# Kernel optimization log

Measured on AMD Instinct MI355X. Metric: run time of the kernel, lower is better.

## Reference

```python
import jax, jax.numpy as jnp
import numpy as np

N = 100000
D = 512   # input_size
C = 2     # output_class
QDIM = 128


def setup_inputs() -> dict:
    key = jax.random.key(0)
    ks = jax.random.split(key, 12)
    s = 0.02
    return {
        "feats": jax.random.normal(ks[0], (N, D), jnp.float32),
        "c": jax.random.normal(ks[1], (N, C), jnp.float32),
        "single_predictions": jax.random.normal(ks[2], (N, 1), jnp.float32),
        # self.lin = Linear(D, D) + ReLU
        "W_lin": jax.random.normal(ks[3], (D, D), jnp.float32) * s,
        "b_lin": jnp.zeros((D,), jnp.float32),
        # self.q = Linear(D, 128) + Tanh
        "W_q": jax.random.normal(ks[4], (QDIM, D), jnp.float32) * s,
        "b_q": jnp.zeros((QDIM,), jnp.float32),
        # self.v = Dropout(0.0) + Linear(D, D)
        "W_v": jax.random.normal(ks[5], (D, D), jnp.float32) * s,
        "b_v": jnp.zeros((D,), jnp.float32),
        # self.fcc = Conv1d(C, C, kernel_size=D)
        "W_fcc": jax.random.normal(ks[6], (C, C, D), jnp.float32) * s,
        "b_fcc": jnp.zeros((C,), jnp.float32),
    }


def reference(feats, c, single_predictions, W_lin, b_lin, W_q, b_q, W_v, b_v, W_fcc, b_fcc):
    n = feats.shape[0]
    k = int(0.2 * n)

    preds = single_predictions[:, 0]                      # [N]
    # torch.topk(largest=False): indices of the k smallest; zero them out
    _, lastk_idx = jax.lax.top_k(-preds, k)
    preds = preds.at[lastk_idx].set(0.0)
    instance_score = jax.nn.softmax(preds, axis=0)[:, None]  # [N,1], softmax over instances

    f = feats * instance_score + feats                    # [N,D]
    f = jax.nn.relu(f @ W_lin.T + b_lin)                  # self.lin
    V = f @ W_v.T + b_v                                   # [N,D] (dropout p=0)
    Q = jnp.tanh(f @ W_q.T + b_q)                         # [N,128]

    # torch.sort(c, 0, descending)[1][0,:] == per-class argmax over instances
    m_indices = jnp.argmax(c, axis=0)                     # [C]
    m_feats = f[m_indices]                                # [C,D]
    q_max = jnp.tanh(m_feats @ W_q.T + b_q)               # [C,128]

    A = Q @ q_max.T                                       # [N,C]
    A = jax.nn.softmax(A / jnp.sqrt(jnp.float32(QDIM)), axis=0)  # softmax over instances
    B = A.T @ V                                           # [C,D]

    # Conv1d(C, C, kernel=D) on B[None] -> length-1 output: full contraction
    Cout = jnp.einsum('id,oid->o', B, W_fcc) + b_fcc      # [C]
    return Cout[None, :], A, B
```

## Files before the change

kernel.cpp:

```cpp
#include <hip/hip_runtime.h>
#include <stdint.h>

typedef unsigned short u16;
typedef __bf16 bf16t;
typedef bf16t bf16x8 __attribute__((ext_vector_type(8)));
typedef float f32x4 __attribute__((ext_vector_type(4)));
typedef unsigned long long ull;

#define NROWS 100000
#define DD 512
#define QD 128
#define KSEL 20000
#define NB 1563

__device__ __forceinline__ uint32_t fmono(float x){
  uint32_t u = __float_as_uint(x);
  return (u & 0x80000000u) ? ~u : (u | 0x80000000u);
}
__device__ __forceinline__ float finv(uint32_t k){
  uint32_t u = (k & 0x80000000u) ? (k & 0x7fffffffu) : ~k;
  return __uint_as_float(u);
}
__device__ __forceinline__ u16 f2bf(float x){
  uint32_t u = __float_as_uint(x);
  u += 0x7fffu + ((u >> 16) & 1u);
  return (u16)(u >> 16);
}
__device__ __forceinline__ uint32_t pkbf(float a, float b){
  return (uint32_t)f2bf(a) | ((uint32_t)f2bf(b) << 16);
}

struct Scal {
  uint32_t keyT;
  float Z;
  uint32_t pad[14];
};

#define MFMA16(A,B,C) __builtin_amdgcn_mfma_f32_16x16x32_bf16(A,B,C,0,0,0)

__global__ void k_conv(const float* __restrict__ Wl, const float* __restrict__ Wv,
                       const float* __restrict__ Wq, u16* __restrict__ wch,
                       uint32_t* __restrict__ hist, ull* __restrict__ cmax){
  int idx = blockIdx.x*256 + threadIdx.x;
  if (idx < 65536) hist[idx] = 0u;
  if (idx == 0){ cmax[0] = 0ull; cmax[1] = 0ull; }
  int ci  = idx >> 12;
  int rem = idx & 4095;
  int r   = rem >> 5;
  int col = rem & 31;
  float v;
  if (ci < 64){
    int nt = ci >> 4, kc = ci & 15;
    v = Wl[(size_t)(nt*128 + r)*DD + kc*32 + col];
  } else {
    int c2 = ci - 64;
    int nt2 = c2 >> 4, kc = c2 & 15;
    if (nt2 == 0) v = Wq[(size_t)r*DD + kc*32 + col];
    else          v = Wv[(size_t)((nt2-1)*128 + r)*DD + kc*32 + col];
  }
  wch[idx] = f2bf(v);
}

__global__ void k_sel1(const float* __restrict__ preds, const float* __restrict__ c,
                       uint32_t* __restrict__ hist, ull* __restrict__ cmax){
  __shared__ ull kr0[4], kr1[4];
  const int t = threadIdx.x;
  const int gid = blockIdx.x*256 + t;
  const int lane = t & 63;

  const float4* p4 = (const float4*)preds;
  for (int i = gid; i < 25000; i += 65536){
    float4 v = p4[i];
    atomicAdd(&hist[fmono(v.x) >> 16], 1u);
    atomicAdd(&hist[fmono(v.y) >> 16], 1u);
    atomicAdd(&hist[fmono(v.z) >> 16], 1u);
    atomicAdd(&hist[fmono(v.w) >> 16], 1u);
  }

  ull k0 = 0ull, k1 = 0ull;
  const float4* c4 = (const float4*)c;
  for (int i = gid; i < 50000; i += 65536){
    float4 v = c4[i];
    uint32_t r0 = 2u*i, r1 = 2u*i + 1u;
    ull a0 = ((ull)fmono(v.x) << 32) | (ull)(~r0);
    ull a1 = ((ull)fmono(v.z) << 32) | (ull)(~r1);
    ull b0 = ((ull)fmono(v.y) << 32) | (ull)(~r0);
    ull b1 = ((ull)fmono(v.w) << 32) | (ull)(~r1);
    if (a0 > k0) k0 = a0;
    if (a1 > k0) k0 = a1;
    if (b0 > k1) k1 = b0;
    if (b1 > k1) k1 = b1;
  }
  #pragma unroll
  for (int off = 32; off; off >>= 1){
    ull o0 = __shfl_xor(k0, off); if (o0 > k0) k0 = o0;
    ull o1 = __shfl_xor(k1, off); if (o1 > k1) k1 = o1;
  }
  if (lane == 0){ kr0[t >> 6] = k0; kr1[t >> 6] = k1; }
  __syncthreads();
  if (t == 0){
    ull m0 = kr0[0], m1 = kr1[0];
    #pragma unroll
    for (int w = 1; w < 4; ++w){
      if (kr0[w] > m0) m0 = kr0[w];
      if (kr1[w] > m1) m1 = kr1[w];
    }
    atomicMax(&cmax[0], m0);
    atomicMax(&cmax[1], m1);
  }
}

#define CAND_CAP 8192
__launch_bounds__(1024)
__global__ void k_prep2(const float* __restrict__ preds,
                        const uint32_t* __restrict__ hist,
                        Scal* __restrict__ sc){
  __shared__ uint32_t cand[CAND_CAP];
  __shared__ uint32_t wsum[16], woff[16];
  __shared__ float zred[16];
  __shared__ uint32_t s_B, s_cumBelow, s_keyT, candN;
  const int t = threadIdx.x;
  const int lane = t & 63, wv = t >> 6;

  if (t == 0) candN = 0;

  const int b0 = t*64;
  uint32_t local = 0;
  {
    const uint4* h4 = (const uint4*)(hist + b0);
    #pragma unroll 4
    for (int q = 0; q < 16; ++q){ uint4 hv = h4[q]; local += hv.x + hv.y + hv.z + hv.w; }
  }
  uint32_t x = local;
  #pragma unroll
  for (int off = 1; off < 64; off <<= 1){
    uint32_t y = __shfl_up(x, off);
    if (lane >= off) x += y;
  }
  if (lane == 63) wsum[wv] = x;
  __syncthreads();
  if (t == 0){
    uint32_t cum = 0;
    for (int w = 0; w < 16; ++w){ woff[w] = cum; cum += wsum[w]; }
  }
  __syncthreads();
  uint32_t excl = x - local + woff[wv];
  if (excl < KSEL && excl + local >= KSEL){
    uint32_t cum = excl;
    for (int b = 0; b < 64; ++b){
      uint32_t h = hist[b0 + b];
      if (cum + h >= KSEL){ s_B = (uint32_t)(b0 + b); s_cumBelow = cum; break; }
      cum += h;
    }
  }
  __syncthreads();
  const uint32_t B = s_B;

  float sA = 0.f;
  const float4* p4 = (const float4*)preds;
  for (int i = t; i < 25000; i += 1024){
    float4 v = p4[i];
    float vv[4] = {v.x, v.y, v.z, v.w};
    #pragma unroll
    for (int e = 0; e < 4; ++e){
      uint32_t k = fmono(vv[e]);
      uint32_t bb = k >> 16;
      if (bb > B){
        sA += __expf(vv[e]);
      } else if (bb == B){
        uint32_t idx = atomicAdd(&candN, 1u);
        if (idx < CAND_CAP) cand[idx] = k;
      }
    }
  }
  #pragma unroll
  for (int off = 32; off; off >>= 1) sA += __shfl_xor(sA, off);
  if (lane == 0) zred[wv] = sA;
  __syncthreads();

  const uint32_t n = candN < CAND_CAP ? candN : CAND_CAP;
  const uint32_t r = KSEL - s_cumBelow;
  for (uint32_t i = t; i < n; i += 1024){
    uint32_t ki = cand[i];
    uint32_t less = 0, eq = 0;
    for (uint32_t j = 0; j < n; ++j){
      uint32_t kj = cand[j];
      less += (kj < ki) ? 1u : 0u;
      eq   += (kj == ki) ? 1u : 0u;
    }
    if (less < r && r <= less + eq) s_keyT = ki;
  }
  __syncthreads();
  const uint32_t keyT = s_keyT;

  float sCA = 0.f;
  for (uint32_t i = t; i < n; i += 1024){
    uint32_t k = cand[i];
    if (k > keyT) sCA += __expf(finv(k));
  }
  #pragma unroll
  for (int off = 32; off; off >>= 1) sCA += __shfl_xor(sCA, off);
  if (lane == 0) zred[wv] += sCA;
  __syncthreads();
  if (t == 0){
    float Z = (float)KSEL;
    for (int w = 0; w < 16; ++w) Z += zred[w];
    sc->keyT = keyT; sc->Z = Z;
  }
}

__global__ void k_prep3(const float* __restrict__ preds, const float* __restrict__ feats,
                        const float* __restrict__ Wl, const float* __restrict__ bl,
                        const ull* __restrict__ cmax, const Scal* __restrict__ sc,
                        float* __restrict__ fmFw){
  __shared__ float fmX[2][512];
  __shared__ uint32_t s_mi[2];
  const int t = threadIdx.x;
  if (t < 2) s_mi[t] = ~(uint32_t)(cmax[t] & 0xffffffffull);
  __syncthreads();
  for (int i = t; i < 1024; i += 256){
    int j = i >> 9, col = i & 511;
    fmX[j][col] = feats[(size_t)s_mi[j]*DD + col];
  }
  __syncthreads();
  const int nn = blockIdx.x*32 + (t >> 3);
  const int h = t & 7;
  const float4* wr4 = (const float4*)(Wl + (size_t)nn*DD + h*64);
  const float4* x04 = (const float4*)(&fmX[0][h*64]);
  const float4* x14 = (const float4*)(&fmX[1][h*64]);
  float a0 = 0.f, a1 = 0.f;
  #pragma unroll
  for (int k = 0; k < 16; ++k){
    float4 w = wr4[k], u = x04[k], v = x14[k];
    a0 += u.x*w.x + u.y*w.y + u.z*w.z + u.w*w.w;
    a1 += v.x*w.x + v.y*w.y + v.z*w.z + v.w*w.w;
  }
  a0 += __shfl_xor(a0, 1); a0 += __shfl_xor(a0, 2); a0 += __shfl_xor(a0, 4);
  a1 += __shfl_xor(a1, 1); a1 += __shfl_xor(a1, 2); a1 += __shfl_xor(a1, 4);
  if (h == 0){
    uint32_t keyT = sc->keyT;
    float Z = sc->Z;
    float p0 = preds[s_mi[0]]; float q0 = (fmono(p0) <= keyT) ? 0.f : p0;
    float g0 = 1.f + __expf(q0) / Z;
    float p1 = preds[s_mi[1]]; float q1 = (fmono(p1) <= keyT) ? 0.f : p1;
    float g1 = 1.f + __expf(q1) / Z;
    float v0 = bl[nn] + g0*a0; fmFw[nn]       = v0 > 0.f ? v0 : 0.f;
    float v1 = bl[nn] + g1*a1; fmFw[512 + nn] = v1 > 0.f ? v1 : 0.f;
  }
}

__global__ void k_prep4(const float* __restrict__ Wq, const float* __restrict__ bq,
                        const float* __restrict__ fmFw, float* __restrict__ qmv){
  __shared__ float xs[512];
  const int t = threadIdx.x;
  const int j = blockIdx.x;
  for (int i = t; i < 512; i += 256) xs[i] = fmFw[j*512 + i];
  __syncthreads();
  const int q = t >> 1, h = t & 1;
  const float4* wr4 = (const float4*)(Wq + (size_t)q*DD + h*256);
  const float4* x4  = (const float4*)(&xs[h*256]);
  float a = 0.f;
  #pragma unroll 4
  for (int k = 0; k < 64; ++k){
    float4 w = wr4[k], u = x4[k];
    a += u.x*w.x + u.y*w.y + u.z*w.z + u.w*w.w;
  }
  a += __shfl_xor(a, 1);
  if (h == 0) qmv[j*QD + q] = tanhf(bq[q] + a);
}

__launch_bounds__(256, 2)
__global__ void k_fused(const float* __restrict__ feats, const float* __restrict__ preds,
                        const u16* __restrict__ wch,
                        const float* __restrict__ bl, const float* __restrict__ bv,
                        const float* __restrict__ bq, const float* __restrict__ qmv,
                        const Scal* __restrict__ sc,
                        float* __restrict__ gpart, float* __restrict__ gpartE,
                        float* __restrict__ Aout){
  __shared__ __align__(16) u16 AF[32768];
  __shared__ __align__(16) float sred[512];
  const int tid = threadIdx.x;
  const int lane = tid & 63, quad = lane >> 4, l16 = lane & 15;
  const int wave = tid >> 6;
  const long i0 = (long)blockIdx.x * 64;
  const uint32_t keyT = sc->keyT;
  const float Z = sc->Z;

  const u16* bsrc = wch + (size_t)((wave*32 + l16)*32 + quad*8);
  uint4 pA0 = *(const uint4*)(bsrc);
  uint4 pA1 = *(const uint4*)(bsrc + 512);
  uint4 pB0 = *(const uint4*)(bsrc + 4096);
  uint4 pB1 = *(const uint4*)(bsrc + 4096 + 512);

  {
    int row = lane;
    long ir = i0 + row; if (ir >= NROWS) ir = NROWS - 1;
    float p = preds[ir];
    float pm = (fmono(p) <= keyT) ? 0.f : p;
    float g = 1.f + __expf(pm) / Z;
    const float4* src = (const float4*)(feats + ir*DD + wave*128);
    u16* dstrow = AF + row*512;
    const int swz = row & 7;
    #pragma unroll
    for (int j = 0; j < 16; ++j){
      float4 a = src[2*j], b = src[2*j + 1];
      uint4 pk;
      pk.x = pkbf(a.x*g, a.y*g); pk.y = pkbf(a.z*g, a.w*g);
      pk.z = pkbf(b.x*g, b.y*g); pk.w = pkbf(b.z*g, b.w*g);
      int blk = (wave << 4) | j;
      *(uint4*)&dstrow[(blk ^ swz) << 3] = pk;
    }
  }
  __syncthreads();

  const int sb = l16 & 7;
  f32x4 acc[4][2];
  uint32_t pkF[4][16];
  float eR0[4][4], eR1[4][4];
  int ci = 0;

#define KSTEP(P0, P1)                                                              \
  {                                                                                \
    bf16x8 b0 = __builtin_bit_cast(bf16x8, P0);                                    \
    bf16x8 b1 = __builtin_bit_cast(bf16x8, P1);                                    \
    if (ci + 2 < 144){                                                             \
      const u16* s_ = bsrc + (size_t)(ci + 2)*4096;                                \
      P0 = *(const uint4*)s_;                                                      \
      P1 = *(const uint4*)(s_ + 512);                                              \
    }                                                                              \
    int abk = ((((ci & 15) << 2) | quad) ^ sb) << 3;                               \
    bf16x8 a0 = *(const bf16x8*)&AF[(     l16)*512 + abk];                         \
    bf16x8 a1 = *(const bf16x8*)&AF[(16 + l16)*512 + abk];                         \
    bf16x8 a2 = *(const bf16x8*)&AF[(32 + l16)*512 + abk];                         \
    bf16x8 a3 = *(const bf16x8*)&AF[(48 + l16)*512 + abk];                         \
    acc[0][0] = MFMA16(a0, b0, acc[0][0]);                                         \
    acc[0][1] = MFMA16(a0, b1, acc[0][1]);                                         \
    acc[1][0] = MFMA16(a1, b0, acc[1][0]);                                         \
    acc[1][1] = MFMA16(a1, b1, acc[1][1]);                                         \
    acc[2][0] = MFMA16(a2, b0, acc[2][0]);                                         \
    acc[2][1] = MFMA16(a2, b1, acc[2][1]);                                         \
    acc[3][0] = MFMA16(a3, b0, acc[3][0]);                                         \
    acc[3][1] = MFMA16(a3, b1, acc[3][1]);                                         \
    ++ci;                                                                          \
  }

  for (int nt = 0; nt < 4; ++nt){
    #pragma unroll
    for (int mi = 0; mi < 4; ++mi)
      #pragma unroll
      for (int ni = 0; ni < 2; ++ni) acc[mi][ni] = (f32x4){0.f,0.f,0.f,0.f};
    for (int kh = 0; kh < 8; ++kh){
      KSTEP(pA0, pA1);
      KSTEP(pB0, pB1);
    }
    #pragma unroll
    for (int ni = 0; ni < 2; ++ni){
      float bb = bl[nt*128 + wave*32 + ni*16 + l16];
      #pragma unroll
      for (int mi = 0; mi < 4; ++mi){
        float e0 = acc[mi][ni][0] + bb; e0 = e0 > 0.f ? e0 : 0.f;
        float e1 = acc[mi][ni][1] + bb; e1 = e1 > 0.f ? e1 : 0.f;
        float e2 = acc[mi][ni][2] + bb; e2 = e2 > 0.f ? e2 : 0.f;
        float e3 = acc[mi][ni][3] + bb; e3 = e3 > 0.f ? e3 : 0.f;
        pkF[nt][mi*4 + ni*2 + 0] = pkbf(e0, e1);
        pkF[nt][mi*4 + ni*2 + 1] = pkbf(e2, e3);
      }
    }
  }

  __syncthreads();
  #pragma unroll
  for (int nt = 0; nt < 4; ++nt)
    #pragma unroll
    for (int mi = 0; mi < 4; ++mi)
      #pragma unroll
      for (int ni = 0; ni < 2; ++ni){
        int col = nt*128 + wave*32 + ni*16 + l16;
        int r0 = mi*16 + quad*4;
        uint32_t x = pkF[nt][mi*4 + ni*2], y = pkF[nt][mi*4 + ni*2 + 1];
        int cb = col >> 3, cw = col & 7;
        AF[(r0+0)*512 + ((cb ^ ((r0+0)&7)) << 3) + cw] = (u16)x;
        AF[(r0+1)*512 + ((cb ^ ((r0+1)&7)) << 3) + cw] = (u16)(x >> 16);
        AF[(r0+2)*512 + ((cb ^ ((r0+2)&7)) << 3) + cw] = (u16)y;
        AF[(r0+3)*512 + ((cb ^ ((r0+3)&7)) << 3) + cw] = (u16)(y >> 16);
      }
  __syncthreads();

  for (int nt2 = 0; nt2 < 5; ++nt2){
    #pragma unroll
    for (int mi = 0; mi < 4; ++mi)
      #pragma unroll
      for (int ni = 0; ni < 2; ++ni) acc[mi][ni] = (f32x4){0.f,0.f,0.f,0.f};
    for (int kh = 0; kh < 8; ++kh){
      KSTEP(pA0, pA1);
      KSTEP(pB0, pB1);
    }
    if (nt2 == 0){
      float p0[4][4], p1[4][4];
      #pragma unroll
      for (int mi = 0; mi < 4; ++mi)
        #pragma unroll
        for (int e = 0; e < 4; ++e){ p0[mi][e] = 0.f; p1[mi][e] = 0.f; }
      #pragma unroll
      for (int ni = 0; ni < 2; ++ni){
        int qc = wave*32 + ni*16 + l16;
        float bqv = bq[qc], q0 = qmv[qc], q1 = qmv[QD + qc];
        #pragma unroll
        for (int mi = 0; mi < 4; ++mi)
          #pragma unroll
          for (int e = 0; e < 4; ++e){
            float tq = tanhf(acc[mi][ni][e] + bqv);
            p0[mi][e] += tq * q0;
            p1[mi][e] += tq * q1;
          }
      }
      #pragma unroll
      for (int off = 1; off <= 8; off <<= 1)
        #pragma unroll
        for (int mi = 0; mi < 4; ++mi)
          #pragma unroll
          for (int e = 0; e < 4; ++e){
            p0[mi][e] += __shfl_xor(p0[mi][e], off);
            p1[mi][e] += __shfl_xor(p1[mi][e], off);
          }
      if (l16 == 0){
        #pragma unroll
        for (int mi = 0; mi < 4; ++mi)
          #pragma unroll
          for (int e = 0; e < 4; ++e){
            int row = mi*16 + quad*4 + e;
            sred[row*8 + 0*4 + wave] = p0[mi][e];
            sred[row*8 + 1*4 + wave] = p1[mi][e];
          }
      }
      __syncthreads();
      #pragma unroll
      for (int mi = 0; mi < 4; ++mi)
        #pragma unroll
        for (int e = 0; e < 4; ++e){
          int row = mi*16 + quad*4 + e;
          bool valid = (i0 + row) < NROWS;
          float sv0 = (sred[row*8+0] + sred[row*8+1] + sred[row*8+2] + sred[row*8+3]) * 0.08838834764831845f;
          float sv1 = (sred[row*8+4] + sred[row*8+5] + sred[row*8+6] + sred[row*8+7]) * 0.08838834764831845f;
          eR0[mi][e] = valid ? __expf(sv0) : 0.f;
          eR1[mi][e] = valid ? __expf(sv1) : 0.f;
        }
      if (tid < 128){
        int row = tid >> 1, j = tid & 1;
        float sv = (sred[row*8 + j*4+0] + sred[row*8 + j*4+1] + sred[row*8 + j*4+2] + sred[row*8 + j*4+3])
                   * 0.08838834764831845f;
        bool valid = (i0 + row) < NROWS;
        float ev = valid ? __expf(sv) : 0.f;
        if (valid) Aout[(i0 + row)*2 + j] = ev;
        float t2 = ev;
        #pragma unroll
        for (int off = 2; off <= 32; off <<= 1) t2 += __shfl_xor(t2, off);
        if (lane < 2) gpartE[(size_t)blockIdx.x*4 + (tid >> 6)*2 + j] = t2;
      }
    } else {
      #pragma unroll
      for (int ni = 0; ni < 2; ++ni){
        int colv = (nt2 - 1)*128 + wave*32 + ni*16 + l16;
        float bvv = bv[colv];
        float b0 = 0.f, b1 = 0.f;
        #pragma unroll
        for (int mi = 0; mi < 4; ++mi)
          #pragma unroll
          for (int e = 0; e < 4; ++e){
            float v = acc[mi][ni][e] + bvv;
            b0 += v * eR0[mi][e];
            b1 += v * eR1[mi][e];
          }
        b0 += __shfl_xor(b0, 16); b0 += __shfl_xor(b0, 32);
        b1 += __shfl_xor(b1, 16); b1 += __shfl_xor(b1, 32);
        if (quad == 0){
          gpart[(size_t)blockIdx.x*1024 + colv]       = b0;
          gpart[(size_t)blockIdx.x*1024 + 512 + colv] = b1;
        }
      }
    }
  }
#undef KSTEP
}

__global__ void k_red(const float* __restrict__ gpart, const float* __restrict__ gpartE,
                      float* __restrict__ sumEV, float* __restrict__ sumE){
  const int t = threadIdx.x;
  if (blockIdx.x == 256){
    __shared__ float r0[256], r1[256];
    float s0 = 0.f, s1 = 0.f;
    for (int i = t; i < NB*2; i += 256){ s0 += gpartE[(size_t)i*2]; s1 += gpartE[(size_t)i*2 + 1]; }
    r0[t] = s0; r1[t] = s1;
    __syncthreads();
    for (int st = 128; st; st >>= 1){
      if (t < st){ r0[t] += r0[t + st]; r1[t] += r1[t + st]; }
      __syncthreads();
    }
    if (t == 0){ sumE[0] = r0[0]; sumE[1] = r1[0]; }
    return;
  }
  __shared__ float4 red[256];
  int col4 = blockIdx.x * 4;
  float4 s = {0.f, 0.f, 0.f, 0.f};
  for (int r = t; r < NB; r += 256){
    float4 v = *(const float4*)(gpart + (size_t)r*1024 + col4);
    s.x += v.x; s.y += v.y; s.z += v.z; s.w += v.w;
  }
  red[t] = s;
  __syncthreads();
  for (int st = 128; st; st >>= 1){
    if (t < st){
      float4 o = red[t + st];
      red[t].x += o.x; red[t].y += o.y; red[t].z += o.z; red[t].w += o.w;
    }
    __syncthreads();
  }
  if (t == 0) *(float4*)(sumEV + col4) = red[0];
}

__global__ void k_post(float* __restrict__ out, const float* __restrict__ sumE,
                       const float* __restrict__ sumEV, const float* __restrict__ Wfcc,
                       const float* __restrict__ bfcc){
  if (blockIdx.x < 782){
    int idx = blockIdx.x*256 + threadIdx.x;
    if (idx < 200000) out[2 + idx] = out[2 + idx] / sumE[idx & 1];
    return;
  }
  __shared__ float red[512];
  int t = threadIdx.x;
  float z0 = sumE[0], z1 = sumE[1];
  float c0 = 0.f, c1 = 0.f;
  for (int e = t; e < 1024; e += 256){
    float bvv = sumEV[e] / ((e >> 9) ? z1 : z0);
    out[200002 + e] = bvv;
    c0 += bvv * Wfcc[e];
    c1 += bvv * Wfcc[1024 + e];
  }
  red[t] = c0; red[256 + t] = c1;
  __syncthreads();
  for (int s = 128; s; s >>= 1){
    if (t < s){ red[t] += red[t + s]; red[256 + t] += red[256 + t + s]; }
    __syncthreads();
  }
  if (t == 0){ out[0] = red[0] + bfcc[0]; out[1] = red[256] + bfcc[1]; }
}

extern "C" void kernel_launch(void* const* d_in, const int* in_sizes, int n_in,
                              void* d_out, int out_size, void* d_ws, size_t ws_size,
                              hipStream_t stream){
  (void)in_sizes; (void)n_in; (void)out_size; (void)ws_size;
  const float* feats = (const float*)d_in[0];
  const float* c     = (const float*)d_in[1];
  const float* preds = (const float*)d_in[2];
  const float* W_lin = (const float*)d_in[3];
  const float* b_lin = (const float*)d_in[4];
  const float* W_q   = (const float*)d_in[5];
  const float* b_q   = (const float*)d_in[6];
  const float* W_v   = (const float*)d_in[7];
  const float* b_v   = (const float*)d_in[8];
  const float* W_fcc = (const float*)d_in[9];
  const float* b_fcc = (const float*)d_in[10];
  float* out = (float*)d_out;
  char* ws = (char*)d_ws;

  u16*   wch    = (u16*)(ws + 0);
  Scal*  sc     = (Scal*)(ws + 1179648);
  float* qmv    = (float*)(ws + 1179712);
  float* sumE   = (float*)(ws + 1180736);
  float* sumEV  = (float*)(ws + 1180800);
  float* fmFw   = (float*)(ws + 1184896);
  float* gpartE = (float*)(ws + 1188992);
  float* gpart  = (float*)(ws + 1214080);
  uint32_t* hist = (uint32_t*)(ws + 1214080);
  ull*      cmax = (ull*)(ws + 1214080 + 262144);

  k_conv <<<2304, 256, 0, stream>>>(W_lin, W_v, W_q, wch, hist, cmax);
  k_sel1 <<<256, 256, 0, stream>>>(preds, c, hist, cmax);
  k_prep2<<<1, 1024, 0, stream>>>(preds, hist, sc);
  k_prep3<<<16, 256, 0, stream>>>(preds, feats, W_lin, b_lin, cmax, sc, fmFw);
  k_prep4<<<2, 256, 0, stream>>>(W_q, b_q, fmFw, qmv);
  k_fused<<<NB, 256, 0, stream>>>(feats, preds, wch, b_lin, b_v, b_q,
                                  qmv, sc, gpart, gpartE, out + 2);
  k_red  <<<257, 256, 0, stream>>>(gpart, gpartE, sumEV, sumE);
  k_post <<<783, 256, 0, stream>>>(out, sumE, sumEV, W_fcc, b_fcc);
}
```

Baseline: 603.6 us.

## Split fused kernel across eight waves and coarsen selection histogram to 4096 bins

```diff
diff --git a/kernel.cpp b/kernel.cpp
--- a/kernel.cpp
+++ b/kernel.cpp
@@ -12,6 +12,7 @@
 #define QD 128
 #define KSEL 20000
 #define NB 1563
+#define NBINS 4096
 
 __device__ __forceinline__ uint32_t fmono(float x){
   uint32_t u = __float_as_uint(x);
@@ -42,7 +43,7 @@
                        const float* __restrict__ Wq, u16* __restrict__ wch,
                        uint32_t* __restrict__ hist, ull* __restrict__ cmax){
   int idx = blockIdx.x*256 + threadIdx.x;
-  if (idx < 65536) hist[idx] = 0u;
+  if (idx < NBINS) hist[idx] = 0u;
   if (idx == 0){ cmax[0] = 0ull; cmax[1] = 0ull; }
   int ci  = idx >> 12;
   int rem = idx & 4095;
@@ -71,10 +72,10 @@
   const float4* p4 = (const float4*)preds;
   for (int i = gid; i < 25000; i += 65536){
     float4 v = p4[i];
-    atomicAdd(&hist[fmono(v.x) >> 16], 1u);
-    atomicAdd(&hist[fmono(v.y) >> 16], 1u);
-    atomicAdd(&hist[fmono(v.z) >> 16], 1u);
-    atomicAdd(&hist[fmono(v.w) >> 16], 1u);
+    atomicAdd(&hist[fmono(v.x) >> 20], 1u);
+    atomicAdd(&hist[fmono(v.y) >> 20], 1u);
+    atomicAdd(&hist[fmono(v.z) >> 20], 1u);
+    atomicAdd(&hist[fmono(v.w) >> 20], 1u);
   }
 
   ull k0 = 0ull, k1 = 0ull;
@@ -124,13 +125,9 @@
 
   if (t == 0) candN = 0;
 
-  const int b0 = t*64;
-  uint32_t local = 0;
-  {
-    const uint4* h4 = (const uint4*)(hist + b0);
-    #pragma unroll 4
-    for (int q = 0; q < 16; ++q){ uint4 hv = h4[q]; local += hv.x + hv.y + hv.z + hv.w; }
-  }
+  const int b0 = t*4;
+  uint4 hv = ((const uint4*)hist)[t];
+  uint32_t local = hv.x + hv.y + hv.z + hv.w;
   uint32_t x = local;
   #pragma unroll
   for (int off = 1; off < 64; off <<= 1){
@@ -147,10 +144,11 @@
   uint32_t excl = x - local + woff[wv];
   if (excl < KSEL && excl + local >= KSEL){
     uint32_t cum = excl;
-    for (int b = 0; b < 64; ++b){
-      uint32_t h = hist[b0 + b];
-      if (cum + h >= KSEL){ s_B = (uint32_t)(b0 + b); s_cumBelow = cum; break; }
-      cum += h;
+    uint32_t hh[4] = {hv.x, hv.y, hv.z, hv.w};
+    #pragma unroll
+    for (int b = 0; b < 4; ++b){
+      if (cum + hh[b] >= KSEL){ s_B = (uint32_t)(b0 + b); s_cumBelow = cum; break; }
+      cum += hh[b];
     }
   }
   __syncthreads();
@@ -164,7 +162,7 @@
     #pragma unroll
     for (int e = 0; e < 4; ++e){
       uint32_t k = fmono(vv[e]);
-      uint32_t bb = k >> 16;
+      uint32_t bb = k >> 20;
       if (bb > B){
         sA += __expf(vv[e]);
       } else if (bb == B){
@@ -269,7 +267,7 @@
   if (h == 0) qmv[j*QD + q] = tanhf(bq[q] + a);
 }
 
-__launch_bounds__(256, 2)
+__launch_bounds__(512, 4)
 __global__ void k_fused(const float* __restrict__ feats, const float* __restrict__ preds,
                         const u16* __restrict__ wch,
                         const float* __restrict__ bl, const float* __restrict__ bv,
@@ -281,12 +279,12 @@
   __shared__ __align__(16) float sred[512];
   const int tid = threadIdx.x;
   const int lane = tid & 63, quad = lane >> 4, l16 = lane & 15;
-  const int wave = tid >> 6;
+  const int wave = tid >> 6, wm = wave >> 2, wn = wave & 3;
   const long i0 = (long)blockIdx.x * 64;
   const uint32_t keyT = sc->keyT;
   const float Z = sc->Z;
 
-  const u16* bsrc = wch + (size_t)((wave*32 + l16)*32 + quad*8);
+  const u16* bsrc = wch + (size_t)((wn*32 + l16)*32 + quad*8);
   uint4 pA0 = *(const uint4*)(bsrc);
   uint4 pA1 = *(const uint4*)(bsrc + 512);
   uint4 pB0 = *(const uint4*)(bsrc + 4096);
@@ -298,66 +296,64 @@
     float p = preds[ir];
     float pm = (fmono(p) <= keyT) ? 0.f : p;
     float g = 1.f + __expf(pm) / Z;
-    const float4* src = (const float4*)(feats + ir*DD + wave*128);
+    const float4* src = (const float4*)(feats + ir*DD + wave*64);
     u16* dstrow = AF + row*512;
     const int swz = row & 7;
     #pragma unroll
-    for (int j = 0; j < 16; ++j){
+    for (int j = 0; j < 8; ++j){
       float4 a = src[2*j], b = src[2*j + 1];
       uint4 pk;
       pk.x = pkbf(a.x*g, a.y*g); pk.y = pkbf(a.z*g, a.w*g);
       pk.z = pkbf(b.x*g, b.y*g); pk.w = pkbf(b.z*g, b.w*g);
-      int blk = (wave << 4) | j;
+      int blk = wave*8 + j;
       *(uint4*)&dstrow[(blk ^ swz) << 3] = pk;
     }
   }
   __syncthreads();
 
   const int sb = l16 & 7;
-  f32x4 acc[4][2];
-  uint32_t pkF[4][16];
-  float eR0[4][4], eR1[4][4];
+  const int base_a0 = (wm*32 + l16) * 512;
+  const int base_a1 = base_a0 + 8192;
+  f32x4 acc[2][2];
+  uint32_t pkF[4][8];
+  float eR0[2][4], eR1[2][4];
   int ci = 0;
 
-#define KSTEP(P0, P1)                                                              \
-  {                                                                                \
-    bf16x8 b0 = __builtin_bit_cast(bf16x8, P0);                                    \
-    bf16x8 b1 = __builtin_bit_cast(bf16x8, P1);                                    \
-    if (ci + 2 < 144){                                                             \
-      const u16* s_ = bsrc + (size_t)(ci + 2)*4096;                                \
-      P0 = *(const uint4*)s_;                                                      \
-      P1 = *(const uint4*)(s_ + 512);                                              \
-    }                                                                              \
-    int abk = ((((ci & 15) << 2) | quad) ^ sb) << 3;                               \
-    bf16x8 a0 = *(const bf16x8*)&AF[(     l16)*512 + abk];                         \
-    bf16x8 a1 = *(const bf16x8*)&AF[(16 + l16)*512 + abk];                         \
-    bf16x8 a2 = *(const bf16x8*)&AF[(32 + l16)*512 + abk];                         \
-    bf16x8 a3 = *(const bf16x8*)&AF[(48 + l16)*512 + abk];                         \
-    acc[0][0] = MFMA16(a0, b0, acc[0][0]);                                         \
-    acc[0][1] = MFMA16(a0, b1, acc[0][1]);                                         \
-    acc[1][0] = MFMA16(a1, b0, acc[1][0]);                                         \
-    acc[1][1] = MFMA16(a1, b1, acc[1][1]);                                         \
-    acc[2][0] = MFMA16(a2, b0, acc[2][0]);                                         \
-    acc[2][1] = MFMA16(a2, b1, acc[2][1]);                                         \
-    acc[3][0] = MFMA16(a3, b0, acc[3][0]);                                         \
-    acc[3][1] = MFMA16(a3, b1, acc[3][1]);                                         \
-    ++ci;                                                                          \
-  }
-
+#define KSTEP(P0, P1)                                                \
+  {                                                                  \
+    bf16x8 b0 = __builtin_bit_cast(bf16x8, P0);                      \
+    bf16x8 b1 = __builtin_bit_cast(bf16x8, P1);                      \
+    if (ci + 2 < 144){                                               \
+      const u16* s_ = bsrc + (size_t)(ci + 2)*4096;                  \
+      P0 = *(const uint4*)s_;                                        \
+      P1 = *(const uint4*)(s_ + 512);                                \
+    }                                                                \
+    int abk = ((((ci & 15) << 2) | quad) ^ sb) << 3;                 \
+    bf16x8 a0 = *(const bf16x8*)&AF[base_a0 + abk];                  \
+    bf16x8 a1 = *(const bf16x8*)&AF[base_a1 + abk];                  \
+    acc[0][0] = MFMA16(a0, b0, acc[0][0]);                           \
+    acc[0][1] = MFMA16(a0, b1, acc[0][1]);                           \
+    acc[1][0] = MFMA16(a1, b0, acc[1][0]);                           \
+    acc[1][1] = MFMA16(a1, b1, acc[1][1]);                           \
+    ++ci;                                                            \
+  }
+
+  #pragma unroll
   for (int nt = 0; nt < 4; ++nt){
     #pragma unroll
-    for (int mi = 0; mi < 4; ++mi)
+    for (int mi = 0; mi < 2; ++mi)
       #pragma unroll
       for (int ni = 0; ni < 2; ++ni) acc[mi][ni] = (f32x4){0.f,0.f,0.f,0.f};
+    #pragma unroll
     for (int kh = 0; kh < 8; ++kh){
       KSTEP(pA0, pA1);
       KSTEP(pB0, pB1);
     }
     #pragma unroll
     for (int ni = 0; ni < 2; ++ni){
-      float bb = bl[nt*128 + wave*32 + ni*16 + l16];
-      #pragma unroll
-      for (int mi = 0; mi < 4; ++mi){
+      float bb = bl[nt*128 + wn*32 + ni*16 + l16];
+      #pragma unroll
+      for (int mi = 0; mi < 2; ++mi){
         float e0 = acc[mi][ni][0] + bb; e0 = e0 > 0.f ? e0 : 0.f;
         float e1 = acc[mi][ni][1] + bb; e1 = e1 > 0.f ? e1 : 0.f;
         float e2 = acc[mi][ni][2] + bb; e2 = e2 > 0.f ? e2 : 0.f;
@@ -372,11 +368,11 @@
   #pragma unroll
   for (int nt = 0; nt < 4; ++nt)
     #pragma unroll
-    for (int mi = 0; mi < 4; ++mi)
+    for (int mi = 0; mi < 2; ++mi)
       #pragma unroll
       for (int ni = 0; ni < 2; ++ni){
-        int col = nt*128 + wave*32 + ni*16 + l16;
-        int r0 = mi*16 + quad*4;
+        int col = nt*128 + wn*32 + ni*16 + l16;
+        int r0 = wm*32 + mi*16 + quad*4;
         uint32_t x = pkF[nt][mi*4 + ni*2], y = pkF[nt][mi*4 + ni*2 + 1];
         int cb = col >> 3, cw = col & 7;
         AF[(r0+0)*512 + ((cb ^ ((r0+0)&7)) << 3) + cw] = (u16)x;
@@ -388,25 +384,26 @@
 
   for (int nt2 = 0; nt2 < 5; ++nt2){
     #pragma unroll
-    for (int mi = 0; mi < 4; ++mi)
+    for (int mi = 0; mi < 2; ++mi)
       #pragma unroll
       for (int ni = 0; ni < 2; ++ni) acc[mi][ni] = (f32x4){0.f,0.f,0.f,0.f};
+    #pragma unroll
     for (int kh = 0; kh < 8; ++kh){
       KSTEP(pA0, pA1);
       KSTEP(pB0, pB1);
     }
     if (nt2 == 0){
-      float p0[4][4], p1[4][4];
-      #pragma unroll
-      for (int mi = 0; mi < 4; ++mi)
+      float p0[2][4], p1[2][4];
+      #pragma unroll
+      for (int mi = 0; mi < 2; ++mi)
         #pragma unroll
         for (int e = 0; e < 4; ++e){ p0[mi][e] = 0.f; p1[mi][e] = 0.f; }
       #pragma unroll
       for (int ni = 0; ni < 2; ++ni){
-        int qc = wave*32 + ni*16 + l16;
+        int qc = wn*32 + ni*16 + l16;
         float bqv = bq[qc], q0 = qmv[qc], q1 = qmv[QD + qc];
         #pragma unroll
-        for (int mi = 0; mi < 4; ++mi)
+        for (int mi = 0; mi < 2; ++mi)
           #pragma unroll
           for (int e = 0; e < 4; ++e){
             float tq = tanhf(acc[mi][ni][e] + bqv);
@@ -417,7 +414,7 @@
       #pragma unroll
       for (int off = 1; off <= 8; off <<= 1)
         #pragma unroll
-        for (int mi = 0; mi < 4; ++mi)
+        for (int mi = 0; mi < 2; ++mi)
           #pragma unroll
           for (int e = 0; e < 4; ++e){
             p0[mi][e] += __shfl_xor(p0[mi][e], off);
@@ -425,20 +422,20 @@
           }
       if (l16 == 0){
         #pragma unroll
-        for (int mi = 0; mi < 4; ++mi)
+        for (int mi = 0; mi < 2; ++mi)
           #pragma unroll
           for (int e = 0; e < 4; ++e){
-            int row = mi*16 + quad*4 + e;
-            sred[row*8 + 0*4 + wave] = p0[mi][e];
-            sred[row*8 + 1*4 + wave] = p1[mi][e];
+            int row = wm*32 + mi*16 + quad*4 + e;
+            sred[row*8 + 0*4 + wn] = p0[mi][e];
+            sred[row*8 + 1*4 + wn] = p1[mi][e];
           }
       }
       __syncthreads();
       #pragma unroll
-      for (int mi = 0; mi < 4; ++mi)
+      for (int mi = 0; mi < 2; ++mi)
         #pragma unroll
         for (int e = 0; e < 4; ++e){
-          int row = mi*16 + quad*4 + e;
+          int row = wm*32 + mi*16 + quad*4 + e;
           bool valid = (i0 + row) < NROWS;
           float sv0 = (sred[row*8+0] + sred[row*8+1] + sred[row*8+2] + sred[row*8+3]) * 0.08838834764831845f;
           float sv1 = (sred[row*8+4] + sred[row*8+5] + sred[row*8+6] + sred[row*8+7]) * 0.08838834764831845f;
@@ -460,11 +457,11 @@
     } else {
       #pragma unroll
       for (int ni = 0; ni < 2; ++ni){
-        int colv = (nt2 - 1)*128 + wave*32 + ni*16 + l16;
+        int colv = (nt2 - 1)*128 + wn*32 + ni*16 + l16;
         float bvv = bv[colv];
         float b0 = 0.f, b1 = 0.f;
         #pragma unroll
-        for (int mi = 0; mi < 4; ++mi)
+        for (int mi = 0; mi < 2; ++mi)
           #pragma unroll
           for (int e = 0; e < 4; ++e){
             float v = acc[mi][ni][e] + bvv;
@@ -474,8 +471,8 @@
         b0 += __shfl_xor(b0, 16); b0 += __shfl_xor(b0, 32);
         b1 += __shfl_xor(b1, 16); b1 += __shfl_xor(b1, 32);
         if (quad == 0){
-          gpart[(size_t)blockIdx.x*1024 + colv]       = b0;
-          gpart[(size_t)blockIdx.x*1024 + 512 + colv] = b1;
+          gpart[((size_t)blockIdx.x*2 + wm)*1024 + colv]       = b0;
+          gpart[((size_t)blockIdx.x*2 + wm)*1024 + 512 + colv] = b1;
         }
       }
     }
@@ -502,7 +499,7 @@
   __shared__ float4 red[256];
   int col4 = blockIdx.x * 4;
   float4 s = {0.f, 0.f, 0.f, 0.f};
-  for (int r = t; r < NB; r += 256){
+  for (int r = t; r < NB*2; r += 256){
     float4 v = *(const float4*)(gpart + (size_t)r*1024 + col4);
     s.x += v.x; s.y += v.y; s.z += v.z; s.w += v.w;
   }
@@ -572,14 +569,14 @@
   float* gpartE = (float*)(ws + 1188992);
   float* gpart  = (float*)(ws + 1214080);
   uint32_t* hist = (uint32_t*)(ws + 1214080);
-  ull*      cmax = (ull*)(ws + 1214080 + 262144);
+  ull*      cmax = (ull*)(ws + 1214080 + 16384);
 
   k_conv <<<2304, 256, 0, stream>>>(W_lin, W_v, W_q, wch, hist, cmax);
   k_sel1 <<<256, 256, 0, stream>>>(preds, c, hist, cmax);
   k_prep2<<<1, 1024, 0, stream>>>(preds, hist, sc);
   k_prep3<<<16, 256, 0, stream>>>(preds, feats, W_lin, b_lin, cmax, sc, fmFw);
   k_prep4<<<2, 256, 0, stream>>>(W_q, b_q, fmFw, qmv);
-  k_fused<<<NB, 256, 0, stream>>>(feats, preds, wch, b_lin, b_v, b_q,
+  k_fused<<<NB, 512, 0, stream>>>(feats, preds, wch, b_lin, b_v, b_q,
                                   qmv, sc, gpart, gpartE, out + 2);
   k_red  <<<257, 256, 0, stream>>>(gpart, gpartE, sumEV, sumE);
   k_post <<<783, 256, 0, stream>>>(out, sumE, sumEV, W_fcc, b_fcc);
```

After: 790.1 us. 30.9% more time.
